# Kernel optimization log

Hardware: AMD Instinct MI355X
Metric: run time of the kernel (lower is better)

The kernel has to match this reference:

```python
import jax, jax.numpy as jnp
import numpy as np
import math

B, S, E, H, L, VOCAB, OUT = 32, 1024, 512, 8, 2, 20000, 1
D = E // H


def positional_encoding(seq_length, embed_size):
    position = jnp.arange(seq_length, dtype=jnp.float32)[:, None]
    div_term = jnp.exp(jnp.arange(0, embed_size, 2, dtype=jnp.float32) * (-math.log(10000.0) / embed_size))
    pe = jnp.zeros((seq_length, embed_size), dtype=jnp.float32)
    pe = pe.at[:, 0::2].set(jnp.sin(position * div_term))
    pe = pe.at[:, 1::2].set(jnp.cos(position * div_term))
    return pe


def setup_inputs() -> dict:
    key = jax.random.key(0)
    ks = jax.random.split(key, 12)
    inputs = jax.random.randint(ks[0], (B, S), 0, VOCAB)
    s = 1.0 / math.sqrt(E)
    embed_table = jax.random.normal(ks[1], (VOCAB, E), jnp.float32)
    embed_table = embed_table.at[0].set(0.0)  # padding_idx=0
    # per-layer Q,K,V,O linear weights [L,E,E] (applied as x @ W + b) and biases [L,E]
    Wq = jax.random.normal(ks[2], (L, E, E), jnp.float32) * s
    Wk = jax.random.normal(ks[3], (L, E, E), jnp.float32) * s
    Wv = jax.random.normal(ks[4], (L, E, E), jnp.float32) * s
    Wo = jax.random.normal(ks[5], (L, E, E), jnp.float32) * s
    bq = jax.random.normal(ks[6], (L, E), jnp.float32) * s
    bk = jax.random.normal(ks[7], (L, E), jnp.float32) * s
    bv = jax.random.normal(ks[8], (L, E), jnp.float32) * s
    bo = jax.random.normal(ks[9], (L, E), jnp.float32) * s
    W_out = jax.random.normal(ks[10], (E, OUT), jnp.float32) * s
    b_out = jax.random.normal(ks[11], (OUT,), jnp.float32) * s
    return {"inputs": inputs, "embed_table": embed_table, "Wq": Wq, "bq": bq,
            "Wk": Wk, "bk": bk, "Wv": Wv, "bv": bv, "Wo": Wo, "bo": bo,
            "W_out": W_out, "b_out": b_out}


def _mha(x, Wq, bq, Wk, bk, Wv, bv, Wo, bo, mask):
    b, s = x.shape[:2]
    def heads(W, bias):
        return (x @ W + bias).reshape(b, s, H, D).transpose(0, 2, 1, 3)  # [b,H,s,D]
    q, k, v = heads(Wq, bq), heads(Wk, bk), heads(Wv, bv)
    scores = jnp.einsum('bhqd,bhkd->bhqk', q, k) / math.sqrt(D)
    scores = jnp.where(mask, -1e9, scores)
    prob = jax.nn.softmax(scores, axis=-1)
    out = jnp.einsum('bhqk,bhkd->bhqd', prob, v)
    out = out.transpose(0, 2, 1, 3).reshape(b, s, E)
    return out @ Wo + bo


def reference(inputs, embed_table, Wq, bq, Wk, bk, Wv, bv, Wo, bo, W_out, b_out):
    embeds = embed_table[inputs]  # [B,S,E]
    embeds = embeds + positional_encoding(inputs.shape[1], embeds.shape[-1])
    mask = jnp.triu(jnp.ones((inputs.shape[1], inputs.shape[1]), bool), k=1)  # future mask
    out = embeds
    for l in range(L):
        attn = _mha(out, Wq[l], bq[l], Wk[l], bk[l], Wv[l], bv[l], Wo[l], bo[l], mask)
        out = out + jax.nn.relu(attn)  # dropout is identity (eval / p=0)
    return out @ W_out + b_out
```

## Files before the change

kernel.cpp:

```cpp
#include <hip/hip_runtime.h>

typedef unsigned short u16;
typedef unsigned int u32;
using short8  = __attribute__((ext_vector_type(8))) short;
using floatx4 = __attribute__((ext_vector_type(4))) float;

#define NB 32
#define SEQ 1024
#define EMB 512
#define NH 8
#define HD 64
#define NLAYER 2
#define M_ROWS (NB * SEQ)

__device__ __forceinline__ float bf2f(u16 u) {
  union { u32 i; float f; } v; v.i = ((u32)u) << 16; return v.f;
}
__device__ __forceinline__ u16 f2bf(float f) {
  union { float f; u32 i; } v; v.f = f;
  u32 r = v.i + 0x7fffu + ((v.i >> 16) & 1u);
  return (u16)(r >> 16);
}

typedef __attribute__((address_space(3))) unsigned int lds_u32_t;
typedef __attribute__((address_space(1))) const unsigned int gbl_u32_t;
__device__ __forceinline__ void gload16(void* lds, const void* g) {
  gbl_u32_t* gp = (gbl_u32_t*)(unsigned long long)g;
  lds_u32_t* lp = (lds_u32_t*)(unsigned int)(unsigned long long)lds;
  __builtin_amdgcn_global_load_lds(gp, lp, 16, 0, 0);
}

__global__ void prep_weights(const float* __restrict__ Wq, const float* __restrict__ Wk,
                             const float* __restrict__ Wv, const float* __restrict__ Wo,
                             u16* __restrict__ WtQKV, u16* __restrict__ WtO) {
  int idx = blockIdx.x * 256 + threadIdx.x;
  const int QKV_TOT = NLAYER * 3 * EMB * EMB;
  if (idx < QKV_TOT) {
    int l = idx / (3 * EMB * EMB);
    int rem = idx % (3 * EMB * EMB);
    int n = rem / EMB, kk = rem % EMB;
    int w = n >> 9, e = n & 511;
    const float* src = (w == 0) ? Wq : (w == 1) ? Wk : Wv;
    WtQKV[idx] = f2bf(src[((size_t)l * EMB + kk) * EMB + e]);
  } else {
    int j = idx - QKV_TOT;
    int l = j / (EMB * EMB);
    int rem = j % (EMB * EMB);
    int n = rem / EMB, kk = rem % EMB;
    WtO[j] = f2bf(Wo[((size_t)l * EMB + kk) * EMB + n]);
  }
}

__global__ void embed_pe(const int* __restrict__ inp, const float* __restrict__ table,
                         u16* __restrict__ x) {
  int row = blockIdx.x;
  int tok = inp[row];
  int s = row & (SEQ - 1);
  const float negln = -9.210340371976184f / (float)EMB;
  for (int e = threadIdx.x; e < EMB; e += blockDim.x) {
    float val = table[(size_t)tok * EMB + e];
    int i = e >> 1;
    float dt = __expf((float)(2 * i) * negln);
    float ang = (float)s * dt;
    float pe = (e & 1) ? __cosf(ang) : __sinf(ang);
    x[(size_t)row * EMB + e] = f2bf(val + pe);
  }
}

#define BK 32

__global__ __launch_bounds__(256) void gemm_bt(
    const u16* __restrict__ A, const u16* __restrict__ Bt, int K, int mode,
    const float* bias0, const float* bias1, const float* bias2,
    u16* out0, u16* out1, u16* out2, const u16* resid, int Nstride) {
  __shared__ u16 sA[2][128][BK];
  __shared__ u16 sB[2][128][BK];
  int tid = threadIdx.x;
  int wave = tid >> 6, lane = tid & 63;
  int quad = lane >> 4, l16 = lane & 15;
  int wm = wave >> 1, wn = wave & 1;

  int NT = (mode == 0) ? 12 : 4;
  int blk = blockIdx.x;
  int xcd = blk & 7, slot = blk >> 3;
  int mtl = slot / NT, ntl = slot % NT;
  int bm0 = (xcd * 32 + mtl) * 128;
  int bn0 = ntl * 128;
  bool vswap = (mode == 0) && (bn0 >= 1024);

  floatx4 acc[4][4];
#pragma unroll
  for (int i = 0; i < 4; ++i)
#pragma unroll
    for (int j = 0; j < 4; ++j) acc[i][j] = (floatx4){0.f, 0.f, 0.f, 0.f};

  int rb = wave * 32;
  int lrow = lane >> 2;
  int gcg = ((lane & 3) ^ ((lane >> 3) & 3)) * 8;
  int rsl = (quad ^ ((l16 >> 1) & 3)) * 8;

  const u16* Arow0 = &A[(size_t)(bm0 + rb + lrow) * K + gcg];
  const u16* Arow1 = &A[(size_t)(bm0 + rb + 16 + lrow) * K + gcg];
  const u16* Brow0 = &Bt[(size_t)(bn0 + rb + lrow) * K + gcg];
  const u16* Brow1 = &Bt[(size_t)(bn0 + rb + 16 + lrow) * K + gcg];

  gload16(&sA[0][rb][0],      Arow0);
  gload16(&sA[0][rb + 16][0], Arow1);
  gload16(&sB[0][rb][0],      Brow0);
  gload16(&sB[0][rb + 16][0], Brow1);

  const int niter = K / BK;
  int ibuf = 0;
  for (int it = 0; it < niter; ++it) {
    if (it + 1 < niter) {
      int k1 = (it + 1) * BK;
      int nb = ibuf ^ 1;
      gload16(&sA[nb][rb][0],      Arow0 + k1);
      gload16(&sA[nb][rb + 16][0], Arow1 + k1);
      gload16(&sB[nb][rb][0],      Brow0 + k1);
      gload16(&sB[nb][rb + 16][0], Brow1 + k1);
      asm volatile("s_waitcnt vmcnt(4)" ::: "memory");
    } else {
      asm volatile("s_waitcnt vmcnt(0)" ::: "memory");
    }
    asm volatile("s_barrier" ::: "memory");

    short8 af[4], bfr[4];
#pragma unroll
    for (int mi = 0; mi < 4; ++mi)
      af[mi] = *(const short8*)&sA[ibuf][wm * 64 + mi * 16 + l16][rsl];
#pragma unroll
    for (int ni = 0; ni < 4; ++ni)
      bfr[ni] = *(const short8*)&sB[ibuf][wn * 64 + ni * 16 + l16][rsl];
    if (!vswap) {
#pragma unroll
      for (int mi = 0; mi < 4; ++mi)
#pragma unroll
        for (int ni = 0; ni < 4; ++ni)
          acc[mi][ni] = __builtin_amdgcn_mfma_f32_16x16x32_bf16(af[mi], bfr[ni], acc[mi][ni], 0, 0, 0);
    } else {
#pragma unroll
      for (int mi = 0; mi < 4; ++mi)
#pragma unroll
        for (int ni = 0; ni < 4; ++ni)
          acc[mi][ni] = __builtin_amdgcn_mfma_f32_16x16x32_bf16(bfr[ni], af[mi], acc[mi][ni], 0, 0, 0);
    }
    asm volatile("s_waitcnt lgkmcnt(0)" ::: "memory");
    asm volatile("s_barrier" ::: "memory");
    ibuf ^= 1;
  }

  u16* scr = ((u16*)sA) + wave * (16 * 68);
  int erow = lane >> 5;
  int dcol = lane & 31;

  if (!vswap) {
    int w = bn0 >> 9;
    const float* bp = (mode == 1) ? bias0 : ((w == 0) ? bias0 : bias1);
    float sc = (mode == 0 && w == 0) ? 0.125f : 1.0f;
    float bv[4];
#pragma unroll
    for (int ni = 0; ni < 4; ++ni)
      bv[ni] = bp[(bn0 + wn * 64 + ni * 16 + l16) & 511];

#pragma unroll
    for (int mi = 0; mi < 4; ++mi) {
#pragma unroll
      for (int ni = 0; ni < 4; ++ni)
#pragma unroll
        for (int r = 0; r < 4; ++r) {
          float t = (acc[mi][ni][r] + bv[ni]) * sc;
          if (mode == 1) t = fmaxf(t, 0.f);
          scr[(quad * 4 + r) * 68 + ni * 16 + l16] = f2bf(t);
        }
      asm volatile("s_waitcnt lgkmcnt(0)" ::: "memory");

      int m0 = bm0 + wm * 64 + mi * 16;
      int colg = bn0 + wn * 64 + dcol * 2;
#pragma unroll
      for (int p = 0; p < 8; ++p) {
        int row = p * 2 + erow;
        u32 d2 = *(const u32*)&scr[row * 68 + dcol * 2];
        int m = m0 + row;
        if (mode == 0) {
          int e = colg & 511, h = e >> 6, d = e & 63;
          int b = m >> 10, sid = m & 1023;
          u16* optr = (w == 0) ? out0 : out1;
          *(u32*)&optr[((size_t)(b * NH + h) * SEQ + sid) * HD + d] = d2;
        } else {
          size_t off = (size_t)m * Nstride + colg;
          u32 rs = *(const u32*)&resid[off];
          float lo = bf2f((u16)d2) + bf2f((u16)rs);
          float hi = bf2f((u16)(d2 >> 16)) + bf2f((u16)(rs >> 16));
          *(u32*)&out0[off] = ((u32)f2bf(hi) << 16) | f2bf(lo);
        }
      }
      asm volatile("s_waitcnt lgkmcnt(0)" ::: "memory");
    }
  } else {
    float bvv[4][4];
#pragma unroll
    for (int ni = 0; ni < 4; ++ni)
#pragma unroll
      for (int r = 0; r < 4; ++r)
        bvv[ni][r] = bias2[(bn0 + wn * 64 + ni * 16 + quad * 4 + r) & 511];

    int b = (bm0 + wm * 64) >> 10;
    int sid0 = (bm0 + wm * 64) & 1023;
    int n0 = bn0 + wn * 64;
    int h = (n0 >> 6) & 7;
#pragma unroll
    for (int ni = 0; ni < 4; ++ni) {
#pragma unroll
      for (int mi = 0; mi < 4; ++mi)
#pragma unroll
        for (int r = 0; r < 4; ++r)
          scr[(quad * 4 + r) * 68 + mi * 16 + l16] = f2bf(acc[mi][ni][r] + bvv[ni][r]);
      asm volatile("s_waitcnt lgkmcnt(0)" ::: "memory");

      int d0 = (n0 & 63) + ni * 16;
#pragma unroll
      for (int p = 0; p < 8; ++p) {
        int row = p * 2 + erow;
        u32 d2 = *(const u32*)&scr[row * 68 + dcol * 2];
        *(u32*)&out2[((size_t)(b * NH + h) * HD + d0 + row) * SEQ + sid0 + dcol * 2] = d2;
      }
      asm volatile("s_waitcnt lgkmcnt(0)" ::: "memory");
    }
  }
}

__device__ __forceinline__ void stage_tile64(u16 (*dst)[64], const u16* g, int gstride,
                                             int wave, int lane) {
  int r = lane >> 3;
  int gcg = ((lane & 7) ^ r) * 8;
#pragma unroll
  for (int c = 0; c < 2; ++c) {
    int row0 = (wave * 2 + c) * 8;
    gload16(&dst[row0][0], &g[(size_t)(row0 + r) * gstride + gcg]);
  }
}
#define RD8(T, row, cg) (*(const short8*)&T[row][(((cg) ^ ((row) & 7)) * 8)])

__global__ __launch_bounds__(256) void attn_kernel(
    const u16* __restrict__ q, const u16* __restrict__ k, const u16* __restrict__ vt,
    u16* __restrict__ o) {
  int blk = blockIdx.x;
  int xcd = blk & 7, slot = blk >> 3;
  int bh = xcd * 32 + (slot >> 3);
  int qtp = slot & 7;
  int b = bh >> 3, h = bh & 7;
  int qA0 = qtp * 128, qB0 = qA0 + 64;
  __shared__ u16 sQ[128][64], sK[64][64], sV[64][64];
  __shared__ u16 sP[2][64][68];
  int tid = threadIdx.x, wave = tid >> 6, lane = tid & 63;
  int quad = lane >> 4, l16 = lane & 15;

  stage_tile64((u16(*)[64])&sQ[0][0],  &q[((size_t)bh * SEQ + qA0) * HD], HD, wave, lane);
  stage_tile64((u16(*)[64])&sQ[64][0], &q[((size_t)bh * SEQ + qB0) * HD], HD, wave, lane);

  short8 ones;
#pragma unroll
  for (int j = 0; j < 8; ++j) ones[j] = (short)0x3F80;

  floatx4 accoA[4], accoB[4], accsumA, accsumB;
#pragma unroll
  for (int i = 0; i < 4; ++i) {
    accoA[i] = (floatx4){0.f, 0.f, 0.f, 0.f};
    accoB[i] = (floatx4){0.f, 0.f, 0.f, 0.f};
  }
  accsumA = (floatx4){0.f, 0.f, 0.f, 0.f};
  accsumB = (floatx4){0.f, 0.f, 0.f, 0.f};
  short8 aqA0 = {}, aqA1 = {}, aqB0 = {}, aqB1 = {};

  auto process = [&](short8 aq0, short8 aq1, int qX0, bool diag, int sub,
                     floatx4* acco, floatx4& accsum, int k0) {
    floatx4 accs[4];
#pragma unroll
    for (int i = 0; i < 4; ++i) accs[i] = (floatx4){0.f, 0.f, 0.f, 0.f};
#pragma unroll
    for (int nt = 0; nt < 4; ++nt) {
      int rbk = nt * 16 + l16;
      accs[nt] = __builtin_amdgcn_mfma_f32_16x16x32_bf16(aq0, RD8(sK, rbk, quad), accs[nt], 0, 0, 0);
      accs[nt] = __builtin_amdgcn_mfma_f32_16x16x32_bf16(aq1, RD8(sK, rbk, 4 + quad), accs[nt], 0, 0, 0);
    }
    int qg_base = qX0 + wave * 16 + quad * 4;
#pragma unroll
    for (int nt = 0; nt < 4; ++nt) {
      int kg = k0 + nt * 16 + l16;
#pragma unroll
      for (int r = 0; r < 4; ++r) {
        float p = __expf(fminf(accs[nt][r], 75.f));
        if (diag && kg > qg_base + r) p = 0.f;
        sP[sub][wave * 16 + quad * 4 + r][nt * 16 + l16] =
            (u16)(__float_as_uint(p) >> 16);
      }
    }
    asm volatile("s_waitcnt lgkmcnt(0)" ::: "memory");
#pragma unroll
    for (int cst = 0; cst < 2; ++cst) {
      short8 ap = *(const short8*)&sP[sub][wave * 16 + l16][cst * 32 + quad * 8];
#pragma unroll
      for (int dt = 0; dt < 4; ++dt) {
        int rv = dt * 16 + l16;
        acco[dt] = __builtin_amdgcn_mfma_f32_16x16x32_bf16(ap, RD8(sV, rv, cst * 4 + quad), acco[dt], 0, 0, 0);
      }
      accsum = __builtin_amdgcn_mfma_f32_16x16x32_bf16(ap, ones, accsum, 0, 0, 0);
    }
  };

  int ktmax = 2 * qtp + 1;
  for (int kt = 0; kt <= ktmax; ++kt) {
    int k0 = kt * 64;
    __syncthreads();
    stage_tile64(sK, &k[((size_t)bh * SEQ + k0) * HD], HD, wave, lane);
    stage_tile64(sV, &vt[(size_t)bh * HD * SEQ + k0], SEQ, wave, lane);
    __syncthreads();

    if (kt == 0) {
      int ra = wave * 16 + l16;
      aqA0 = RD8(sQ, ra, quad);
      aqA1 = RD8(sQ, ra, 4 + quad);
      int rb_ = 64 + wave * 16 + l16;
      aqB0 = RD8(sQ, rb_, quad);
      aqB1 = RD8(sQ, rb_, 4 + quad);
    }

    if (kt <= 2 * qtp)
      process(aqA0, aqA1, qA0, kt == 2 * qtp, 0, accoA, accsumA, k0);
    process(aqB0, aqB1, qB0, kt == ktmax, 1, accoB, accsumB, k0);
  }

#pragma unroll
  for (int dt = 0; dt < 4; ++dt)
#pragma unroll
    for (int r = 0; r < 4; ++r) {
      int rowoff = wave * 16 + quad * 4 + r;
      int col = h * HD + dt * 16 + l16;
      o[((size_t)b * SEQ + qA0 + rowoff) * EMB + col] = f2bf(accoA[dt][r] / accsumA[r]);
      o[((size_t)b * SEQ + qB0 + rowoff) * EMB + col] = f2bf(accoB[dt][r] / accsumB[r]);
    }
}

__global__ __launch_bounds__(256) void out_proj(const u16* __restrict__ x,
                                                const float* __restrict__ wout,
                                                const float* __restrict__ bout,
                                                float* __restrict__ out) {
  int wave = threadIdx.x >> 6, lane = threadIdx.x & 63;
  int m = blockIdx.x * 4 + wave;
  union { uint4 vv; u16 s[8]; } xv;
  xv.vv = *(const uint4*)&x[(size_t)m * EMB + lane * 8];
  float4 w0 = *(const float4*)&wout[lane * 8];
  float4 w1 = *(const float4*)&wout[lane * 8 + 4];
  float wv[8] = {w0.x, w0.y, w0.z, w0.w, w1.x, w1.y, w1.z, w1.w};
  float s = 0.f;
#pragma unroll
  for (int j = 0; j < 8; ++j) s += bf2f(xv.s[j]) * wv[j];
#pragma unroll
  for (int sh = 1; sh < 64; sh <<= 1) s += __shfl_xor(s, sh, 64);
  if (lane == 0) out[m] = s + bout[0];
}

extern "C" void kernel_launch(void* const* d_in, const int* in_sizes, int n_in,
                              void* d_out, int out_size, void* d_ws, size_t ws_size,
                              hipStream_t stream) {
  const int*   inp   = (const int*)d_in[0];
  const float* table = (const float*)d_in[1];
  const float* Wq    = (const float*)d_in[2];
  const float* bq    = (const float*)d_in[3];
  const float* Wk    = (const float*)d_in[4];
  const float* bk    = (const float*)d_in[5];
  const float* Wv    = (const float*)d_in[6];
  const float* bv    = (const float*)d_in[7];
  const float* Wo    = (const float*)d_in[8];
  const float* bo    = (const float*)d_in[9];
  const float* Wout  = (const float*)d_in[10];
  const float* bout  = (const float*)d_in[11];
  float* outp = (float*)d_out;

  char* ws = (char*)d_ws;
  const size_t SZ = (size_t)M_ROWS * EMB * 2;
  u16* x      = (u16*)(ws);
  u16* qb     = (u16*)(ws + SZ);
  u16* kb     = (u16*)(ws + 2 * SZ);
  u16* vb     = (u16*)(ws + 3 * SZ);
  u16* attn_b = (u16*)(ws + 4 * SZ);
  u16* WtQKV  = (u16*)(ws + 5 * SZ);
  u16* WtO    = (u16*)(ws + 5 * SZ + (size_t)NLAYER * 3 * EMB * EMB * 2);

  prep_weights<<<8192, 256, 0, stream>>>(Wq, Wk, Wv, Wo, WtQKV, WtO);
  embed_pe<<<M_ROWS, 256, 0, stream>>>(inp, table, x);

  for (int l = 0; l < NLAYER; ++l) {
    gemm_bt<<<3072, 256, 0, stream>>>(
        x, WtQKV + (size_t)l * 3 * EMB * EMB, EMB, 0,
        bq + l * EMB, bk + l * EMB, bv + l * EMB, qb, kb, vb, nullptr, 0);
    attn_kernel<<<2048, 256, 0, stream>>>(qb, kb, vb, attn_b);
    gemm_bt<<<1024, 256, 0, stream>>>(
        attn_b, WtO + (size_t)l * EMB * EMB, EMB, 1,
        bo + l * EMB, nullptr, nullptr, x, nullptr, nullptr, x, EMB);
  }
  out_proj<<<8192, 256, 0, stream>>>(x, Wout, bout, outp);
}
```

Measured before the change: 641.9 us.

## Widen GEMM tiles to 128x256 and double-buffer K/V tiles in attention

The GEMM kernel's N tile grows from 128 to 256. Each wave now holds a 4x8 accumulator array and the grid halves, so each A tile loaded from global memory feeds twice as many MFMAs. The epilogues write the wider tile in two halves. Separately, the attention kernel gains double-buffered K/V shared tiles so the next tile's global loads overlap the current tile's compute, replacing the two syncthreads per iteration with waitcnt and barrier pairs. In exchange, register and LDS use both rise, which may lower occupancy.

```diff
diff --git a/kernel.cpp b/kernel.cpp
--- a/kernel.cpp
+++ b/kernel.cpp
@@ -74,40 +74,43 @@
     const float* bias0, const float* bias1, const float* bias2,
     u16* out0, u16* out1, u16* out2, const u16* resid, int Nstride) {
   __shared__ u16 sA[2][128][BK];
-  __shared__ u16 sB[2][128][BK];
+  __shared__ u16 sB[2][256][BK];
   int tid = threadIdx.x;
   int wave = tid >> 6, lane = tid & 63;
   int quad = lane >> 4, l16 = lane & 15;
   int wm = wave >> 1, wn = wave & 1;
 
-  int NT = (mode == 0) ? 12 : 4;
+  int NT2 = (mode == 0) ? 6 : 2;
   int blk = blockIdx.x;
   int xcd = blk & 7, slot = blk >> 3;
-  int mtl = slot / NT, ntl = slot % NT;
+  int mtl = slot / NT2, ntl = slot % NT2;
   int bm0 = (xcd * 32 + mtl) * 128;
-  int bn0 = ntl * 128;
+  int bn0 = ntl * 256;
   bool vswap = (mode == 0) && (bn0 >= 1024);
 
-  floatx4 acc[4][4];
+  floatx4 acc[4][8];
 #pragma unroll
   for (int i = 0; i < 4; ++i)
 #pragma unroll
-    for (int j = 0; j < 4; ++j) acc[i][j] = (floatx4){0.f, 0.f, 0.f, 0.f};
-
-  int rb = wave * 32;
+    for (int j = 0; j < 8; ++j) acc[i][j] = (floatx4){0.f, 0.f, 0.f, 0.f};
+
+  int rbA = wave * 32;
+  int rbB = wave * 64;
   int lrow = lane >> 2;
   int gcg = ((lane & 3) ^ ((lane >> 3) & 3)) * 8;
   int rsl = (quad ^ ((l16 >> 1) & 3)) * 8;
 
-  const u16* Arow0 = &A[(size_t)(bm0 + rb + lrow) * K + gcg];
-  const u16* Arow1 = &A[(size_t)(bm0 + rb + 16 + lrow) * K + gcg];
-  const u16* Brow0 = &Bt[(size_t)(bn0 + rb + lrow) * K + gcg];
-  const u16* Brow1 = &Bt[(size_t)(bn0 + rb + 16 + lrow) * K + gcg];
-
-  gload16(&sA[0][rb][0],      Arow0);
-  gload16(&sA[0][rb + 16][0], Arow1);
-  gload16(&sB[0][rb][0],      Brow0);
-  gload16(&sB[0][rb + 16][0], Brow1);
+  const u16* Arow0 = &A[(size_t)(bm0 + rbA + lrow) * K + gcg];
+  const u16* Arow1 = &A[(size_t)(bm0 + rbA + 16 + lrow) * K + gcg];
+  const u16* Brow[4];
+#pragma unroll
+  for (int c = 0; c < 4; ++c)
+    Brow[c] = &Bt[(size_t)(bn0 + rbB + c * 16 + lrow) * K + gcg];
+
+  gload16(&sA[0][rbA][0],      Arow0);
+  gload16(&sA[0][rbA + 16][0], Arow1);
+#pragma unroll
+  for (int c = 0; c < 4; ++c) gload16(&sB[0][rbB + c * 16][0], Brow[c]);
 
   const int niter = K / BK;
   int ibuf = 0;
@@ -115,34 +118,34 @@
     if (it + 1 < niter) {
       int k1 = (it + 1) * BK;
       int nb = ibuf ^ 1;
-      gload16(&sA[nb][rb][0],      Arow0 + k1);
-      gload16(&sA[nb][rb + 16][0], Arow1 + k1);
-      gload16(&sB[nb][rb][0],      Brow0 + k1);
-      gload16(&sB[nb][rb + 16][0], Brow1 + k1);
-      asm volatile("s_waitcnt vmcnt(4)" ::: "memory");
+      gload16(&sA[nb][rbA][0],      Arow0 + k1);
+      gload16(&sA[nb][rbA + 16][0], Arow1 + k1);
+#pragma unroll
+      for (int c = 0; c < 4; ++c) gload16(&sB[nb][rbB + c * 16][0], Brow[c] + k1);
+      asm volatile("s_waitcnt vmcnt(6)" ::: "memory");
     } else {
       asm volatile("s_waitcnt vmcnt(0)" ::: "memory");
     }
     asm volatile("s_barrier" ::: "memory");
 
-    short8 af[4], bfr[4];
+    short8 af[4], bfr[8];
 #pragma unroll
     for (int mi = 0; mi < 4; ++mi)
       af[mi] = *(const short8*)&sA[ibuf][wm * 64 + mi * 16 + l16][rsl];
 #pragma unroll
-    for (int ni = 0; ni < 4; ++ni)
-      bfr[ni] = *(const short8*)&sB[ibuf][wn * 64 + ni * 16 + l16][rsl];
+    for (int ni = 0; ni < 8; ++ni)
+      bfr[ni] = *(const short8*)&sB[ibuf][wn * 128 + ni * 16 + l16][rsl];
     if (!vswap) {
 #pragma unroll
       for (int mi = 0; mi < 4; ++mi)
 #pragma unroll
-        for (int ni = 0; ni < 4; ++ni)
+        for (int ni = 0; ni < 8; ++ni)
           acc[mi][ni] = __builtin_amdgcn_mfma_f32_16x16x32_bf16(af[mi], bfr[ni], acc[mi][ni], 0, 0, 0);
     } else {
 #pragma unroll
       for (int mi = 0; mi < 4; ++mi)
 #pragma unroll
-        for (int ni = 0; ni < 4; ++ni)
+        for (int ni = 0; ni < 8; ++ni)
           acc[mi][ni] = __builtin_amdgcn_mfma_f32_16x16x32_bf16(bfr[ni], af[mi], acc[mi][ni], 0, 0, 0);
     }
     asm volatile("s_waitcnt lgkmcnt(0)" ::: "memory");
@@ -158,67 +161,67 @@
     int w = bn0 >> 9;
     const float* bp = (mode == 1) ? bias0 : ((w == 0) ? bias0 : bias1);
     float sc = (mode == 0 && w == 0) ? 0.125f : 1.0f;
-    float bv[4];
-#pragma unroll
-    for (int ni = 0; ni < 4; ++ni)
-      bv[ni] = bp[(bn0 + wn * 64 + ni * 16 + l16) & 511];
+    float bv[8];
+#pragma unroll
+    for (int ni = 0; ni < 8; ++ni)
+      bv[ni] = bp[(bn0 + wn * 128 + ni * 16 + l16) & 511];
 
 #pragma unroll
     for (int mi = 0; mi < 4; ++mi) {
 #pragma unroll
-      for (int ni = 0; ni < 4; ++ni)
+      for (int half = 0; half < 2; ++half) {
+#pragma unroll
+        for (int ni4 = 0; ni4 < 4; ++ni4) {
+          int ni = half * 4 + ni4;
+#pragma unroll
+          for (int r = 0; r < 4; ++r) {
+            float t = (acc[mi][ni][r] + bv[ni]) * sc;
+            if (mode == 1) t = fmaxf(t, 0.f);
+            scr[(quad * 4 + r) * 68 + ni4 * 16 + l16] = f2bf(t);
+          }
+        }
+        asm volatile("s_waitcnt lgkmcnt(0)" ::: "memory");
+
+        int m0 = bm0 + wm * 64 + mi * 16;
+        int colg = bn0 + wn * 128 + half * 64 + dcol * 2;
+#pragma unroll
+        for (int p = 0; p < 8; ++p) {
+          int row = p * 2 + erow;
+          u32 d2 = *(const u32*)&scr[row * 68 + dcol * 2];
+          int m = m0 + row;
+          if (mode == 0) {
+            int e = colg & 511, h = e >> 6, d = e & 63;
+            int b = m >> 10, sid = m & 1023;
+            u16* optr = (w == 0) ? out0 : out1;
+            *(u32*)&optr[((size_t)(b * NH + h) * SEQ + sid) * HD + d] = d2;
+          } else {
+            size_t off = (size_t)m * Nstride + colg;
+            u32 rs = *(const u32*)&resid[off];
+            float lo = bf2f((u16)d2) + bf2f((u16)rs);
+            float hi = bf2f((u16)(d2 >> 16)) + bf2f((u16)(rs >> 16));
+            *(u32*)&out0[off] = ((u32)f2bf(hi) << 16) | f2bf(lo);
+          }
+        }
+        asm volatile("s_waitcnt lgkmcnt(0)" ::: "memory");
+      }
+    }
+  } else {
+    int b = (bm0 + wm * 64) >> 10;
+    int sid0 = (bm0 + wm * 64) & 1023;
+    int n0 = bn0 + wn * 128;
+#pragma unroll
+    for (int ni = 0; ni < 8; ++ni) {
+#pragma unroll
+      for (int mi = 0; mi < 4; ++mi)
 #pragma unroll
         for (int r = 0; r < 4; ++r) {
-          float t = (acc[mi][ni][r] + bv[ni]) * sc;
-          if (mode == 1) t = fmaxf(t, 0.f);
-          scr[(quad * 4 + r) * 68 + ni * 16 + l16] = f2bf(t);
+          float t = acc[mi][ni][r] + bias2[(n0 + ni * 16 + quad * 4 + r) & 511];
+          scr[(quad * 4 + r) * 68 + mi * 16 + l16] = f2bf(t);
         }
       asm volatile("s_waitcnt lgkmcnt(0)" ::: "memory");
 
-      int m0 = bm0 + wm * 64 + mi * 16;
-      int colg = bn0 + wn * 64 + dcol * 2;
-#pragma unroll
-      for (int p = 0; p < 8; ++p) {
-        int row = p * 2 + erow;
-        u32 d2 = *(const u32*)&scr[row * 68 + dcol * 2];
-        int m = m0 + row;
-        if (mode == 0) {
-          int e = colg & 511, h = e >> 6, d = e & 63;
-          int b = m >> 10, sid = m & 1023;
-          u16* optr = (w == 0) ? out0 : out1;
-          *(u32*)&optr[((size_t)(b * NH + h) * SEQ + sid) * HD + d] = d2;
-        } else {
-          size_t off = (size_t)m * Nstride + colg;
-          u32 rs = *(const u32*)&resid[off];
-          float lo = bf2f((u16)d2) + bf2f((u16)rs);
-          float hi = bf2f((u16)(d2 >> 16)) + bf2f((u16)(rs >> 16));
-          *(u32*)&out0[off] = ((u32)f2bf(hi) << 16) | f2bf(lo);
-        }
-      }
-      asm volatile("s_waitcnt lgkmcnt(0)" ::: "memory");
-    }
-  } else {
-    float bvv[4][4];
-#pragma unroll
-    for (int ni = 0; ni < 4; ++ni)
-#pragma unroll
-      for (int r = 0; r < 4; ++r)
-        bvv[ni][r] = bias2[(bn0 + wn * 64 + ni * 16 + quad * 4 + r) & 511];
-
-    int b = (bm0 + wm * 64) >> 10;
-    int sid0 = (bm0 + wm * 64) & 1023;
-    int n0 = bn0 + wn * 64;
-    int h = (n0 >> 6) & 7;
-#pragma unroll
-    for (int ni = 0; ni < 4; ++ni) {
-#pragma unroll
-      for (int mi = 0; mi < 4; ++mi)
-#pragma unroll
-        for (int r = 0; r < 4; ++r)
-          scr[(quad * 4 + r) * 68 + mi * 16 + l16] = f2bf(acc[mi][ni][r] + bvv[ni][r]);
-      asm volatile("s_waitcnt lgkmcnt(0)" ::: "memory");
-
-      int d0 = (n0 & 63) + ni * 16;
+      int h = ((n0 + ni * 16) >> 6) & 7;
+      int d0 = (ni & 3) * 16;
 #pragma unroll
       for (int p = 0; p < 8; ++p) {
         int row = p * 2 + erow;
@@ -251,13 +254,16 @@
   int qtp = slot & 7;
   int b = bh >> 3, h = bh & 7;
   int qA0 = qtp * 128, qB0 = qA0 + 64;
-  __shared__ u16 sQ[128][64], sK[64][64], sV[64][64];
+  __shared__ u16 sQ[128][64];
+  __shared__ u16 sK[2][64][64], sV[2][64][64];
   __shared__ u16 sP[2][64][68];
   int tid = threadIdx.x, wave = tid >> 6, lane = tid & 63;
   int quad = lane >> 4, l16 = lane & 15;
 
   stage_tile64((u16(*)[64])&sQ[0][0],  &q[((size_t)bh * SEQ + qA0) * HD], HD, wave, lane);
   stage_tile64((u16(*)[64])&sQ[64][0], &q[((size_t)bh * SEQ + qB0) * HD], HD, wave, lane);
+  stage_tile64(sK[0], &k[(size_t)bh * SEQ * HD], HD, wave, lane);
+  stage_tile64(sV[0], &vt[(size_t)bh * HD * SEQ], SEQ, wave, lane);
 
   short8 ones;
 #pragma unroll
@@ -273,7 +279,7 @@
   accsumB = (floatx4){0.f, 0.f, 0.f, 0.f};
   short8 aqA0 = {}, aqA1 = {}, aqB0 = {}, aqB1 = {};
 
-  auto process = [&](short8 aq0, short8 aq1, int qX0, bool diag, int sub,
+  auto process = [&](short8 aq0, short8 aq1, int qX0, bool diag, int sub, int ib,
                      floatx4* acco, floatx4& accsum, int k0) {
     floatx4 accs[4];
 #pragma unroll
@@ -281,8 +287,8 @@
 #pragma unroll
     for (int nt = 0; nt < 4; ++nt) {
       int rbk = nt * 16 + l16;
-      accs[nt] = __builtin_amdgcn_mfma_f32_16x16x32_bf16(aq0, RD8(sK, rbk, quad), accs[nt], 0, 0, 0);
-      accs[nt] = __builtin_amdgcn_mfma_f32_16x16x32_bf16(aq1, RD8(sK, rbk, 4 + quad), accs[nt], 0, 0, 0);
+      accs[nt] = __builtin_amdgcn_mfma_f32_16x16x32_bf16(aq0, RD8(sK[ib], rbk, quad), accs[nt], 0, 0, 0);
+      accs[nt] = __builtin_amdgcn_mfma_f32_16x16x32_bf16(aq1, RD8(sK[ib], rbk, 4 + quad), accs[nt], 0, 0, 0);
     }
     int qg_base = qX0 + wave * 16 + quad * 4;
 #pragma unroll
@@ -303,19 +309,25 @@
 #pragma unroll
       for (int dt = 0; dt < 4; ++dt) {
         int rv = dt * 16 + l16;
-        acco[dt] = __builtin_amdgcn_mfma_f32_16x16x32_bf16(ap, RD8(sV, rv, cst * 4 + quad), acco[dt], 0, 0, 0);
+        acco[dt] = __builtin_amdgcn_mfma_f32_16x16x32_bf16(ap, RD8(sV[ib], rv, cst * 4 + quad), acco[dt], 0, 0, 0);
       }
       accsum = __builtin_amdgcn_mfma_f32_16x16x32_bf16(ap, ones, accsum, 0, 0, 0);
     }
   };
 
   int ktmax = 2 * qtp + 1;
+  int ibuf = 0;
   for (int kt = 0; kt <= ktmax; ++kt) {
     int k0 = kt * 64;
-    __syncthreads();
-    stage_tile64(sK, &k[((size_t)bh * SEQ + k0) * HD], HD, wave, lane);
-    stage_tile64(sV, &vt[(size_t)bh * HD * SEQ + k0], SEQ, wave, lane);
-    __syncthreads();
+    if (kt < ktmax) {
+      int nb = ibuf ^ 1;
+      stage_tile64(sK[nb], &k[((size_t)bh * SEQ + k0 + 64) * HD], HD, wave, lane);
+      stage_tile64(sV[nb], &vt[(size_t)bh * HD * SEQ + k0 + 64], SEQ, wave, lane);
+      asm volatile("s_waitcnt vmcnt(4)" ::: "memory");
+    } else {
+      asm volatile("s_waitcnt vmcnt(0)" ::: "memory");
+    }
+    asm volatile("s_barrier" ::: "memory");
 
     if (kt == 0) {
       int ra = wave * 16 + l16;
@@ -327,8 +339,12 @@
     }
 
     if (kt <= 2 * qtp)
-      process(aqA0, aqA1, qA0, kt == 2 * qtp, 0, accoA, accsumA, k0);
-    process(aqB0, aqB1, qB0, kt == ktmax, 1, accoB, accsumB, k0);
+      process(aqA0, aqA1, qA0, kt == 2 * qtp, 0, ibuf, accoA, accsumA, k0);
+    process(aqB0, aqB1, qB0, kt == ktmax, 1, ibuf, accoB, accsumB, k0);
+
+    asm volatile("s_waitcnt lgkmcnt(0)" ::: "memory");
+    asm volatile("s_barrier" ::: "memory");
+    ibuf ^= 1;
   }
 
 #pragma unroll
@@ -392,11 +408,11 @@
   embed_pe<<<M_ROWS, 256, 0, stream>>>(inp, table, x);
 
   for (int l = 0; l < NLAYER; ++l) {
-    gemm_bt<<<3072, 256, 0, stream>>>(
+    gemm_bt<<<1536, 256, 0, stream>>>(
         x, WtQKV + (size_t)l * 3 * EMB * EMB, EMB, 0,
         bq + l * EMB, bk + l * EMB, bv + l * EMB, qb, kb, vb, nullptr, 0);
     attn_kernel<<<2048, 256, 0, stream>>>(qb, kb, vb, attn_b);
-    gemm_bt<<<1024, 256, 0, stream>>>(
+    gemm_bt<<<512, 256, 0, stream>>>(
         attn_b, WtO + (size_t)l * EMB * EMB, EMB, 1,
         bo + l * EMB, nullptr, nullptr, x, nullptr, nullptr, x, EMB);
   }
```

Measured after the change: 834.1 us. 29.9% more time.
